# Optimization experiments

Measured on AMD Instinct MI355X. Metric: run time of the kernel, lower is better.

## Reference

```python
import jax, jax.numpy as jnp
import numpy as np

B, Q, S, U = 65536, 128, 8, 32  # batch, n_slices, slice_length (1024/128), hidden units


def setup_inputs() -> dict:
    key = jax.random.key(0)
    k1, k2, k3 = jax.random.split(key, 3)
    x = jax.random.normal(k1, (B, 1, 1, Q * S), dtype=jnp.float32)
    # Per-slice 2-layer MLP params: Dense(U, elu) then Dense(1), one set per slice.
    W1 = jax.random.normal(k2, (Q, S, U), dtype=jnp.float32) * (1.0 / np.sqrt(S))
    b1 = jnp.zeros((Q, U), dtype=jnp.float32)
    W2 = jax.random.normal(k3, (Q, U, 1), dtype=jnp.float32) * (1.0 / np.sqrt(U))
    b2 = jnp.zeros((Q, 1), dtype=jnp.float32)
    return {"x": x, "W1": W1, "b1": b1, "W2": W2, "b2": b2}


def reference(x, W1, b1, W2, b2):
    # x: (B,1,1,C) -> (B, Q, S); note: BN layers in the original __init__ are
    # never used in call(), so the forward is purely the per-slice MLPs.
    b = x.shape[0]
    xs = jnp.reshape(x, (b, Q, S))
    # All 128 per-slice Dense layers fused into one batched GEMM.
    h = jax.nn.elu(jnp.einsum('bqs,qsu->bqu', xs, W1) + b1)  # (B,Q,U)
    out = jnp.einsum('bqu,quo->bqo', h, W2) + b2              # (B,Q,1)
    return jnp.reshape(out, (b, Q))                           # concat over q -> (B,Q)
```

## Files before the change

### kernel.cpp

```cpp
#include <hip/hip_runtime.h>

#define Q    128
#define S    8
#define U    32
#define QW   8
#define TROWS 64
#define RPB  1024
#define NTILE (RPB / TROWS)
#define RSTRIDE 144
#define XSBUF (TROWS * RSTRIDE)
#define ZOFF  (2 * XSBUF)
#define OSS   20
#define OSBUF (TROWS * OSS)

typedef __attribute__((ext_vector_type(8)))  __bf16 bf16x8;
typedef __attribute__((ext_vector_type(16))) float  f32x16;
typedef __attribute__((ext_vector_type(2)))  float  f32x2;

__device__ inline unsigned short f2bf(float f) {
    unsigned int u = __float_as_uint(f);
    u += 0x7FFF + ((u >> 16) & 1);
    return (unsigned short)(u >> 16);
}

__device__ inline unsigned int cvt_pk_bf16(float lo, float hi) {
    unsigned int r;
    asm("v_cvt_pk_bf16_f32 %0, %1, %2" : "=v"(r) : "v"(lo), "v"(hi));
    return r;
}

__global__ void prep_kernel(const float* __restrict__ W1, const float* __restrict__ b1,
                            const float* __restrict__ W2, const float* __restrict__ b2,
                            unsigned short* __restrict__ W1T,
                            float* __restrict__ b1F, float* __restrict__ w2F,
                            float* __restrict__ b2F)
{
    const int q = blockIdx.x, t = threadIdx.x;
    const int u = t & 31, s = t >> 5;
    W1T[(q * 32 + u) * 8 + s] = f2bf(W1[(q * 8 + s) * 32 + u]);
    if (t < 32) {
        int reg = t & 15, hh = t >> 4;
        int uu  = (reg & 3) + 8 * (reg >> 2) + 4 * hh;
        b1F[(q * 2 + hh) * 16 + reg] = b1[q * 32 + uu] + 1.0f;
        w2F[(q * 2 + hh) * 16 + reg] = W2[q * 32 + uu];
    }
    if (t == 0) {
        float sw = 0.f;
        for (int uu = 0; uu < 32; ++uu) sw += W2[q * 32 + uu];
        b2F[q] = b2[q] - sw;
    }
}

__global__ __launch_bounds__(256)
__attribute__((amdgpu_waves_per_eu(3, 4)))
void divenc_wreg(const float* __restrict__ x,
                 const unsigned short* __restrict__ W1T,
                 const float* __restrict__ b1F,
                 const float* __restrict__ w2F,
                 const float* __restrict__ b2F,
                 float* __restrict__ out, int B)
{
    __shared__ __align__(16) unsigned char xs[2 * XSBUF + 16];
    __shared__ __align__(16) float os[2 * OSBUF];

    const int t    = threadIdx.x;
    const int lane = t & 63;
    const int wv   = __builtin_amdgcn_readfirstlane(t >> 6);
    const int bl   = lane & 31;
    const int h    = lane >> 5;
    const bool lo  = (lane < 32);

    const int bid   = blockIdx.x;
    const int qb    = (bid & 15) * QW;
    const int rbase = (bid >> 4) * RPB;
    const int rmax  = B - 1;

    if (t == 0) *(uint4*)(xs + ZOFF) = uint4{0, 0, 0, 0};

    const int qA = qb + wv * 2, qB = qA + 1;
    const uint4  axA  = *(const uint4*)(W1T + ((size_t)qA * 32 + bl) * 8);
    const uint4  axB  = *(const uint4*)(W1T + ((size_t)qB * 32 + bl) * 8);
    const f32x16 cinA = *(const f32x16*)(b1F + ((size_t)qA * 2 + h) * 16);
    const f32x16 cinB = *(const f32x16*)(b1F + ((size_t)qB * 2 + h) * 16);
    const f32x16 wrA  = *(const f32x16*)(w2F + ((size_t)qA * 2 + h) * 16);
    const f32x16 wrB  = *(const f32x16*)(w2F + ((size_t)qB * 2 + h) * 16);
    const float  b2A  = b2F[qA], b2B = b2F[qB];

    const f32x2 l2e2  = 1.44269504088896f;
    const f32x2 nl2e2 = -1.44269504088896f;
    const f32x2 zero2 = 0.0f;

    const int row0 = t >> 3,          qr0 = t & 7;
    const int row1 = (t + 256) >> 3,  qr1 = t & 7;
    float4 pa0, pb0, pa1, pb1;

#define LOADT(T) {                                                                   \
    int r0_ = rbase + (T) * TROWS + row0; if (r0_ > rmax) r0_ = rmax;                \
    int r1_ = rbase + (T) * TROWS + row1; if (r1_ > rmax) r1_ = rmax;                \
    const float4* p0_ = (const float4*)(x + (size_t)r0_ * (Q * S)                    \
                                          + (size_t)(qb + qr0) * S);                 \
    const float4* p1_ = (const float4*)(x + (size_t)r1_ * (Q * S)                    \
                                          + (size_t)(qb + qr1) * S);                 \
    pa0 = p0_[0]; pb0 = p0_[1];                                                      \
    pa1 = p1_[0]; pb1 = p1_[1]; }

#define WRITET(BUF) {                                                                \
    uint4 w0_, w1_;                                                                  \
    w0_.x = cvt_pk_bf16(pa0.x, pa0.y); w0_.y = cvt_pk_bf16(pa0.z, pa0.w);            \
    w0_.z = cvt_pk_bf16(pb0.x, pb0.y); w0_.w = cvt_pk_bf16(pb0.z, pb0.w);            \
    w1_.x = cvt_pk_bf16(pa1.x, pa1.y); w1_.y = cvt_pk_bf16(pa1.z, pa1.w);            \
    w1_.z = cvt_pk_bf16(pb1.x, pb1.y); w1_.w = cvt_pk_bf16(pb1.z, pb1.w);            \
    *(uint4*)(xs + (BUF) * XSBUF + row0 * RSTRIDE + qr0 * 16) = w0_;                 \
    *(uint4*)(xs + (BUF) * XSBUF + row1 * RSTRIDE + qr1 * 16) = w1_; }

#define EL2(CC, J, WR, ACC) {                                                        \
    f32x2 v_; v_.x = CC[2*(J)]; v_.y = CC[2*(J)+1];                                  \
    f32x2 w2v; w2v.x = WR[2*(J)]; w2v.y = WR[2*(J)+1];                               \
    f32x2 f_ = __builtin_elementwise_fma(v_, l2e2, nl2e2);                           \
    f_ = __builtin_elementwise_min(f_, zero2);                                       \
    f32x2 e_; e_.x = __builtin_amdgcn_exp2f(f_.x);                                   \
    e_.y = __builtin_amdgcn_exp2f(f_.y);                                             \
    f32x2 r_ = __builtin_elementwise_max(v_, e_);                                    \
    ACC = __builtin_elementwise_fma(r_, w2v, ACC); }

#define COMP(AX, CIN, WR, B2, QR, RBUF, OSP) {                                       \
    const int xoff = (RBUF) + bl * RSTRIDE + (QR) * 16;                              \
    uint4 bx0 = *(const uint4*)(xs + (lo ? xoff                : ZOFF));             \
    uint4 bx1 = *(const uint4*)(xs + (lo ? xoff + 32 * RSTRIDE : ZOFF));             \
    f32x16 cc0 = __builtin_amdgcn_mfma_f32_32x32x16_bf16(                            \
        __builtin_bit_cast(bf16x8, AX), __builtin_bit_cast(bf16x8, bx0),             \
        CIN, 0, 0, 0);                                                               \
    f32x16 cc1 = __builtin_amdgcn_mfma_f32_32x32x16_bf16(                            \
        __builtin_bit_cast(bf16x8, AX), __builtin_bit_cast(bf16x8, bx1),             \
        CIN, 0, 0, 0);                                                               \
    f32x2 acc0 = 0.0f, acc1 = 0.0f;                                                  \
    EL2(cc0, 0, WR, acc0) EL2(cc0, 1, WR, acc0) EL2(cc0, 2, WR, acc0)                \
    EL2(cc0, 3, WR, acc0) EL2(cc0, 4, WR, acc0) EL2(cc0, 5, WR, acc0)                \
    EL2(cc0, 6, WR, acc0) EL2(cc0, 7, WR, acc0)                                      \
    EL2(cc1, 0, WR, acc1) EL2(cc1, 1, WR, acc1) EL2(cc1, 2, WR, acc1)                \
    EL2(cc1, 3, WR, acc1) EL2(cc1, 4, WR, acc1) EL2(cc1, 5, WR, acc1)                \
    EL2(cc1, 6, WR, acc1) EL2(cc1, 7, WR, acc1)                                      \
    float a0 = acc0.x + acc0.y;                                                      \
    float a1 = acc1.x + acc1.y;                                                      \
    a0 += __shfl_xor(a0, 32);                                  \
    a1 += __shfl_xor(a1, 32);                                                        \
    if (lo) {                                                                        \
        os[(OSP) + bl * OSS + (QR)]        = a0 + (B2);                              \
        os[(OSP) + (bl + 32) * OSS + (QR)] = a1 + (B2);                              \
    } }

#define STORE(T, OSP) {                                                              \
    if (t < 128) {                                                                   \
        int row_ = t >> 1, c_ = t & 1;                                               \
        float4 o_ = *(const float4*)&os[(OSP) + row_ * OSS + c_ * 4];                \
        int r_ = rbase + (T) * TROWS + row_;                                         \
        if (r_ < B)                                                                  \
            *(float4*)(out + (size_t)r_ * Q + qb + c_ * 4) = o_;                     \
    } }

    LOADT(0) WRITET(0)

    #pragma unroll 1
    for (int tile = 0; tile < NTILE; ++tile) {
        __syncthreads();
        const int rbuf = (tile & 1) * XSBUF;
        const int osp  = (tile & 1) * OSBUF;
        const int psp  = ((tile & 1) ^ 1) * OSBUF;

        if (tile + 1 < NTILE) LOADT(tile + 1)
        if (tile > 0)         STORE(tile - 1, psp)

        COMP(axA, cinA, wrA, b2A, wv * 2,     rbuf, osp)
        COMP(axB, cinB, wrB, b2B, wv * 2 + 1, rbuf, osp)

        if (tile + 1 < NTILE) WRITET((tile + 1) & 1)
    }
    __syncthreads();
    STORE(NTILE - 1, ((NTILE - 1) & 1) * OSBUF)
#undef LOADT
#undef WRITET
#undef EL2
#undef COMP
#undef STORE
}

extern "C" void kernel_launch(void* const* d_in, const int* in_sizes, int n_in,
                              void* d_out, int out_size, void* d_ws, size_t ws_size,
                              hipStream_t stream) {
    const float* x  = (const float*)d_in[0];
    const float* W1 = (const float*)d_in[1];
    const float* b1 = (const float*)d_in[2];
    const float* W2 = (const float*)d_in[3];
    const float* b2 = (const float*)d_in[4];
    float* out = (float*)d_out;

    unsigned short* W1T = (unsigned short*)d_ws;
    float*          b1F = (float*)((char*)d_ws + 65536);
    float*          w2F = (float*)((char*)d_ws + 81920);
    float*          b2F = (float*)((char*)d_ws + 98304);

    const int B = in_sizes[0] / (Q * S);
    const int nblocks = ((B + RPB - 1) / RPB) * (Q / QW);

    hipLaunchKernelGGL(prep_kernel, dim3(Q), dim3(256), 0, stream,
                       W1, b1, W2, b2, W1T, b1F, w2F, b2F);
    hipLaunchKernelGGL(divenc_wreg, dim3(nblocks), dim3(256), 0, stream,
                       x, W1T, b1F, w2F, b2F, out, B);
}
```

Before: 89.86 us.

## Deepen global-load prefetch to two tiles ahead and single-buffer output staging

New measurement: 82.78 us. -7.9%, faster.

```diff
diff --git a/kernel.cpp b/kernel.cpp
--- a/kernel.cpp
+++ b/kernel.cpp
@@ -7,11 +7,10 @@
 #define TROWS 64
 #define RPB  1024
 #define NTILE (RPB / TROWS)
-#define RSTRIDE 144
+#define RSTRIDE 272
 #define XSBUF (TROWS * RSTRIDE)
 #define ZOFF  (2 * XSBUF)
-#define OSS   20
-#define OSBUF (TROWS * OSS)
+#define OSS  20
 
 typedef __attribute__((ext_vector_type(8)))  __bf16 bf16x8;
 typedef __attribute__((ext_vector_type(16))) float  f32x16;
@@ -53,15 +52,12 @@
 
 __global__ __launch_bounds__(256)
 __attribute__((amdgpu_waves_per_eu(3, 4)))
-void divenc_wreg(const float* __restrict__ x,
-                 const unsigned short* __restrict__ W1T,
-                 const float* __restrict__ b1F,
-                 const float* __restrict__ w2F,
-                 const float* __restrict__ b2F,
-                 float* __restrict__ out, int B)
+void divenc_pipe(const float* __restrict__ x, const unsigned short* __restrict__ W1T,
+                 const float* __restrict__ b1F, const float* __restrict__ w2F,
+                 const float* __restrict__ b2F, float* __restrict__ out, int B)
 {
     __shared__ __align__(16) unsigned char xs[2 * XSBUF + 16];
-    __shared__ __align__(16) float os[2 * OSBUF];
+    __shared__ __align__(16) float os[TROWS * OSS];
 
     const int t    = threadIdx.x;
     const int lane = t & 63;
@@ -69,7 +65,6 @@
     const int bl   = lane & 31;
     const int h    = lane >> 5;
     const bool lo  = (lane < 32);
-
     const int bid   = blockIdx.x;
     const int qb    = (bid & 15) * QW;
     const int rbase = (bid >> 4) * RPB;
@@ -90,8 +85,8 @@
     const f32x2 nl2e2 = -1.44269504088896f;
     const f32x2 zero2 = 0.0f;
 
-    const int row0 = t >> 3,          qr0 = t & 7;
-    const int row1 = (t + 256) >> 3,  qr1 = t & 7;
+    const int row0 = t >> 3,         qr0 = t & 7;
+    const int row1 = (t + 256) >> 3, qr1 = t & 7;
     float4 pa0, pb0, pa1, pb1;
 
 #define LOADT(T) {                                                                   \
@@ -104,14 +99,14 @@
     pa0 = p0_[0]; pb0 = p0_[1];                                                      \
     pa1 = p1_[0]; pb1 = p1_[1]; }
 
-#define WRITET(BUF) {                                                                \
+#define WRITET(XB) {                                                                 \
     uint4 w0_, w1_;                                                                  \
     w0_.x = cvt_pk_bf16(pa0.x, pa0.y); w0_.y = cvt_pk_bf16(pa0.z, pa0.w);            \
     w0_.z = cvt_pk_bf16(pb0.x, pb0.y); w0_.w = cvt_pk_bf16(pb0.z, pb0.w);            \
     w1_.x = cvt_pk_bf16(pa1.x, pa1.y); w1_.y = cvt_pk_bf16(pa1.z, pa1.w);            \
     w1_.z = cvt_pk_bf16(pb1.x, pb1.y); w1_.w = cvt_pk_bf16(pb1.z, pb1.w);            \
-    *(uint4*)(xs + (BUF) * XSBUF + row0 * RSTRIDE + qr0 * 16) = w0_;                 \
-    *(uint4*)(xs + (BUF) * XSBUF + row1 * RSTRIDE + qr1 * 16) = w1_; }
+    *(uint4*)(xs + (XB) + row0 * RSTRIDE + qr0 * 16) = w0_;                          \
+    *(uint4*)(xs + (XB) + row1 * RSTRIDE + qr1 * 16) = w1_; }
 
 #define EL2(CC, J, WR, ACC) {                                                        \
     f32x2 v_; v_.x = CC[2*(J)]; v_.y = CC[2*(J)+1];                                  \
@@ -123,8 +118,8 @@
     f32x2 r_ = __builtin_elementwise_max(v_, e_);                                    \
     ACC = __builtin_elementwise_fma(r_, w2v, ACC); }
 
-#define COMP(AX, CIN, WR, B2, QR, RBUF, OSP) {                                       \
-    const int xoff = (RBUF) + bl * RSTRIDE + (QR) * 16;                              \
+#define COMP(AX, CIN, WR, B2, QR, XB) {                                              \
+    const int xoff = (XB) + bl * RSTRIDE + (QR) * 16;                                \
     uint4 bx0 = *(const uint4*)(xs + (lo ? xoff                : ZOFF));             \
     uint4 bx1 = *(const uint4*)(xs + (lo ? xoff + 32 * RSTRIDE : ZOFF));             \
     f32x16 cc0 = __builtin_amdgcn_mfma_f32_32x32x16_bf16(                            \
@@ -142,41 +137,35 @@
     EL2(cc1, 6, WR, acc1) EL2(cc1, 7, WR, acc1)                                      \
     float a0 = acc0.x + acc0.y;                                                      \
     float a1 = acc1.x + acc1.y;                                                      \
-    a0 += __shfl_xor(a0, 32);                                  \
+    a0 += __shfl_xor(a0, 32);                                                        \
     a1 += __shfl_xor(a1, 32);                                                        \
     if (lo) {                                                                        \
-        os[(OSP) + bl * OSS + (QR)]        = a0 + (B2);                              \
-        os[(OSP) + (bl + 32) * OSS + (QR)] = a1 + (B2);                              \
+        os[bl * OSS + (QR)]        = a0 + (B2);                                      \
+        os[(bl + 32) * OSS + (QR)] = a1 + (B2);                                      \
     } }
 
-#define STORE(T, OSP) {                                                              \
+#define STORE(T) {                                                                   \
     if (t < 128) {                                                                   \
         int row_ = t >> 1, c_ = t & 1;                                               \
-        float4 o_ = *(const float4*)&os[(OSP) + row_ * OSS + c_ * 4];                \
+        float4 o_ = *(const float4*)&os[row_ * OSS + c_ * 4];                        \
         int r_ = rbase + (T) * TROWS + row_;                                         \
         if (r_ < B)                                                                  \
             *(float4*)(out + (size_t)r_ * Q + qb + c_ * 4) = o_;                     \
     } }
 
     LOADT(0) WRITET(0)
+    LOADT(1)
 
     #pragma unroll 1
     for (int tile = 0; tile < NTILE; ++tile) {
         __syncthreads();
-        const int rbuf = (tile & 1) * XSBUF;
-        const int osp  = (tile & 1) * OSBUF;
-        const int psp  = ((tile & 1) ^ 1) * OSBUF;
-
-        if (tile + 1 < NTILE) LOADT(tile + 1)
-        if (tile > 0)         STORE(tile - 1, psp)
-
-        COMP(axA, cinA, wrA, b2A, wv * 2,     rbuf, osp)
-        COMP(axB, cinB, wrB, b2B, wv * 2 + 1, rbuf, osp)
-
-        if (tile + 1 < NTILE) WRITET((tile + 1) & 1)
+        if (tile + 1 < NTILE) WRITET(((tile + 1) & 1) * XSBUF)
+        if (tile + 2 < NTILE) LOADT(tile + 2)
+        COMP(axA, cinA, wrA, b2A, wv * 2,     (tile & 1) * XSBUF)
+        COMP(axB, cinB, wrB, b2B, wv * 2 + 1, (tile & 1) * XSBUF)
+        __syncthreads();
+        STORE(tile)
     }
-    __syncthreads();
-    STORE(NTILE - 1, ((NTILE - 1) & 1) * OSBUF)
 #undef LOADT
 #undef WRITET
 #undef EL2
@@ -204,6 +193,6 @@
 
     hipLaunchKernelGGL(prep_kernel, dim3(Q), dim3(256), 0, stream,
                        W1, b1, W2, b2, W1T, b1F, w2F, b2F);
-    hipLaunchKernelGGL(divenc_wreg, dim3(nblocks), dim3(256), 0, stream,
+    hipLaunchKernelGGL(divenc_pipe, dim3(nblocks), dim3(256), 0, stream,
                        x, W1T, b1F, w2F, b2F, out, B);
 }
```
